# Kernel optimization log

Hardware: AMD Instinct MI355X
Metric: run time of the kernel (lower is better)

## Reference

```python
import jax, jax.numpy as jnp
import numpy as np

H = 4096  # hidden_size == input_size


def setup_inputs() -> dict:
    key = jax.random.key(0)
    ks = jax.random.split(key, 12)
    s = 0.02  # weight init scale
    return {
        "x": jax.random.normal(ks[0], (H,), jnp.float32),
        "h_prev": jnp.zeros((H,), jnp.float32),
        "C_prev": jax.random.normal(ks[1], (H, H), jnp.float32) * 0.01,
        "n_prev": jax.random.uniform(ks[2], (H,), jnp.float32) + 1.0,
        # projection weights (hidden_size x input_size) and biases
        "Wq": jax.random.normal(ks[3], (H, H), jnp.float32) * s,
        "Wk": jax.random.normal(ks[4], (H, H), jnp.float32) * s,
        "Wv": jax.random.normal(ks[5], (H, H), jnp.float32) * s,
        "Wo": jax.random.normal(ks[6], (H, H), jnp.float32) * s,
        "bq": jnp.zeros((H,), jnp.float32),
        "bk": jnp.zeros((H,), jnp.float32),
        "bv": jnp.zeros((H,), jnp.float32),
        "bo": jnp.zeros((H,), jnp.float32),
        # scalar input/forget gates: w^T x + b
        "wi": jax.random.normal(ks[7], (H,), jnp.float32) * s,
        "bi": jnp.zeros((), jnp.float32),
        "wf": jax.random.normal(ks[8], (H,), jnp.float32) * s,
        "bf": jnp.ones((), jnp.float32),  # bias forget gate toward remembering
    }


def reference(x, h_prev, C_prev, n_prev, Wq, Wk, Wv, Wo,
              bq, bk, bv, bo, wi, bi, wf, bf):
    # mLSTM single-step cell (xLSTM matrix memory). h_prev is unused by the
    # mLSTM math (no hidden-to-hidden recurrence), matching the CUDA layer API.
    d = jnp.asarray(Wk.shape[0], x.dtype)
    q = Wq @ x + bq                                   # [H]
    k = (Wk @ x + bk) / jnp.sqrt(d)                   # [H], scaled key
    v = Wv @ x + bv                                   # [H]
    i_gate = jnp.exp(jnp.dot(wi, x) + bi)             # scalar exponential input gate
    f_gate = jax.nn.sigmoid(jnp.dot(wf, x) + bf)      # scalar sigmoid forget gate
    # covariance-style rank-1 matrix-memory update
    C = f_gate * C_prev + i_gate * jnp.outer(v, k)    # [H, H]
    n = f_gate * n_prev + i_gate * k                  # [H]
    # normalized readout
    denom = jnp.maximum(jnp.abs(jnp.dot(n, q)), jnp.asarray(1.0, x.dtype))
    h_tilde = (C @ q) / denom                         # [H]
    o_gate = jax.nn.sigmoid(Wo @ x + bo)              # [H] output gate
    h = o_gate * h_tilde
    return (h, C, n)
```

## Files before the change

### kernel.cpp

```cpp
#include <hip/hip_runtime.h>
#include <math.h>

#define H 4096
#define H4 (H / 4)

typedef float f4 __attribute__((ext_vector_type(4)));

__device__ __forceinline__ float wave_reduce_sum(float v) {
    #pragma unroll
    for (int off = 32; off > 0; off >>= 1)
        v += __shfl_down(v, off, 64);
    return v;
}

__device__ __forceinline__ float sigmoidf_(float x) {
    return 1.0f / (1.0f + __expf(-x));
}

__device__ __forceinline__ float dot4(f4 a, f4 b) {
    return a.x * b.x + a.y * b.y + a.z * b.z + a.w * b.w;
}

__global__ __launch_bounds__(1024) void gemv_all(
    const float* __restrict__ x,
    const float* __restrict__ Wq, const float* __restrict__ Wk,
    const float* __restrict__ Wv, const float* __restrict__ Wo,
    const float* __restrict__ bq, const float* __restrict__ bk,
    const float* __restrict__ bv, const float* __restrict__ bo,
    const float* __restrict__ wi, const float* __restrict__ wf,
    float* __restrict__ q, float* __restrict__ k,
    float* __restrict__ v, float* __restrict__ og,
    float* __restrict__ s2)
{
    const int tid  = threadIdx.x;
    const int wave = tid >> 6;
    const int lane = tid & 63;

    __shared__ f4 xs[H4];
    const f4* x4 = (const f4*)x;
    xs[tid] = x4[tid];
    __syncthreads();

    const int rowId = blockIdx.x * 16 + wave;
    if (rowId >= 4 * H + 2) return;

    const int m = rowId >> 12;
    const int r = rowId & (H - 1);

    const float* row;
    if (rowId < 4 * H) {
        const float* W = (m == 0) ? Wq : (m == 1) ? Wk : (m == 2) ? Wv : Wo;
        row = W + (size_t)r * H;
    } else {
        row = (rowId == 4 * H) ? wi : wf;
    }
    const f4* row4 = (const f4*)row;

    float s = 0.0f;
    #pragma unroll
    for (int half = 0; half < 2; ++half) {
        const int base = half * 512;
        f4 a0 = __builtin_nontemporal_load(&row4[lane + base +   0]);
        f4 a1 = __builtin_nontemporal_load(&row4[lane + base +  64]);
        f4 a2 = __builtin_nontemporal_load(&row4[lane + base + 128]);
        f4 a3 = __builtin_nontemporal_load(&row4[lane + base + 192]);
        f4 a4_ = __builtin_nontemporal_load(&row4[lane + base + 256]);
        f4 a5 = __builtin_nontemporal_load(&row4[lane + base + 320]);
        f4 a6 = __builtin_nontemporal_load(&row4[lane + base + 384]);
        f4 a7 = __builtin_nontemporal_load(&row4[lane + base + 448]);
        s += dot4(a0,  xs[lane + base +   0]);
        s += dot4(a1,  xs[lane + base +  64]);
        s += dot4(a2,  xs[lane + base + 128]);
        s += dot4(a3,  xs[lane + base + 192]);
        s += dot4(a4_, xs[lane + base + 256]);
        s += dot4(a5,  xs[lane + base + 320]);
        s += dot4(a6,  xs[lane + base + 384]);
        s += dot4(a7,  xs[lane + base + 448]);
    }

    s = wave_reduce_sum(s);

    if (lane == 0) {
        if (rowId < 4 * H) {
            if (m == 0)      q[r]  = s + bq[r];
            else if (m == 1) k[r]  = (s + bk[r]) * 0.015625f;
            else if (m == 2) v[r]  = s + bv[r];
            else             og[r] = sigmoidf_(s + bo[r]);
        } else {
            s2[rowId - 4 * H] = s;
        }
    }
}

__global__ __launch_bounds__(256) void c_update(
    const float* __restrict__ C_prev,
    const float* __restrict__ q, const float* __restrict__ k,
    const float* __restrict__ v, const float* __restrict__ s2,
    const float* __restrict__ bi, const float* __restrict__ bf,
    float* __restrict__ C_out, float* __restrict__ u)
{
    const int tid  = threadIdx.x;
    const int wave = tid >> 6;
    const int lane = tid & 63;

    __shared__ f4 qs[H4];
    __shared__ f4 ks[H4];
    const f4* q4 = (const f4*)q;
    const f4* k4 = (const f4*)k;
    #pragma unroll
    for (int i = 0; i < 4; ++i) {
        qs[tid + i * 256] = q4[tid + i * 256];
        ks[tid + i * 256] = k4[tid + i * 256];
    }
    __syncthreads();

    const int r = blockIdx.x * 4 + wave;

    const float ig  = __expf(s2[0] + bi[0]);
    const float fg  = sigmoidf_(s2[1] + bf[0]);
    const float ivr = ig * v[r];

    const f4* c4 = (const f4*)(C_prev + (size_t)r * H);
    f4*       o4 = (f4*)(C_out + (size_t)r * H);

    float acc = 0.0f;
    #pragma unroll
    for (int half = 0; half < 2; ++half) {
        const int base = half * 512;
        f4 a0 = __builtin_nontemporal_load(&c4[lane + base +   0]);
        f4 a1 = __builtin_nontemporal_load(&c4[lane + base +  64]);
        f4 a2 = __builtin_nontemporal_load(&c4[lane + base + 128]);
        f4 a3 = __builtin_nontemporal_load(&c4[lane + base + 192]);
        f4 a4_ = __builtin_nontemporal_load(&c4[lane + base + 256]);
        f4 a5 = __builtin_nontemporal_load(&c4[lane + base + 320]);
        f4 a6 = __builtin_nontemporal_load(&c4[lane + base + 384]);
        f4 a7 = __builtin_nontemporal_load(&c4[lane + base + 448]);

        f4 o;
        #define CONSUME(reg, off)                                        \
            {                                                            \
                f4 kk = ks[lane + (off)];                                \
                o.x = fg * reg.x + ivr * kk.x;                           \
                o.y = fg * reg.y + ivr * kk.y;                           \
                o.z = fg * reg.z + ivr * kk.z;                           \
                o.w = fg * reg.w + ivr * kk.w;                           \
                __builtin_nontemporal_store(o, &o4[lane + (off)]);       \
                acc += dot4(reg, qs[lane + (off)]);                      \
            }
        CONSUME(a0, base +   0) CONSUME(a1, base +  64)
        CONSUME(a2, base + 128) CONSUME(a3, base + 192)
        CONSUME(a4_, base + 256) CONSUME(a5, base + 320)
        CONSUME(a6, base + 384) CONSUME(a7, base + 448)
        #undef CONSUME
    }

    acc = wave_reduce_sum(acc);
    if (lane == 0) u[r] = acc;
}

__global__ __launch_bounds__(1024) void finalize(
    const float* __restrict__ n_prev,
    const float* __restrict__ q, const float* __restrict__ k,
    const float* __restrict__ v, const float* __restrict__ og,
    const float* __restrict__ u, const float* __restrict__ s2,
    const float* __restrict__ bi, const float* __restrict__ bf,
    float* __restrict__ h, float* __restrict__ n_out)
{
    const int t = threadIdx.x;
    const int wave = t >> 6;
    const int lane = t & 63;

    const float ig = __expf(s2[0] + bi[0]);
    const float fg = sigmoidf_(s2[1] + bf[0]);

    float nq = 0.0f, kq = 0.0f;
    for (int j = t; j < H; j += 1024) {
        float kj = k[j];
        float qj = q[j];
        float nj = fg * n_prev[j] + ig * kj;
        n_out[j] = nj;
        nq += nj * qj;
        kq += kj * qj;
    }
    nq = wave_reduce_sum(nq);
    kq = wave_reduce_sum(kq);

    __shared__ float snq[16], skq[16];
    if (lane == 0) { snq[wave] = nq; skq[wave] = kq; }
    __syncthreads();
    if (t == 0) {
        float a = 0.0f, b = 0.0f;
        #pragma unroll
        for (int w = 0; w < 16; ++w) { a += snq[w]; b += skq[w]; }
        snq[0] = a; skq[0] = b;
    }
    __syncthreads();

    const float denom = fmaxf(fabsf(snq[0]), 1.0f);
    const float kqv = skq[0];
    const float inv_denom = 1.0f / denom;

    for (int j = t; j < H; j += 1024) {
        float ht = (fg * u[j] + ig * v[j] * kqv) * inv_denom;
        h[j] = og[j] * ht;
    }
}

extern "C" void kernel_launch(void* const* d_in, const int* in_sizes, int n_in,
                              void* d_out, int out_size, void* d_ws, size_t ws_size,
                              hipStream_t stream) {
    const float* x      = (const float*)d_in[0];
    const float* C_prev = (const float*)d_in[2];
    const float* n_prev = (const float*)d_in[3];
    const float* Wq     = (const float*)d_in[4];
    const float* Wk     = (const float*)d_in[5];
    const float* Wv     = (const float*)d_in[6];
    const float* Wo     = (const float*)d_in[7];
    const float* bq     = (const float*)d_in[8];
    const float* bk     = (const float*)d_in[9];
    const float* bv     = (const float*)d_in[10];
    const float* bo     = (const float*)d_in[11];
    const float* wi     = (const float*)d_in[12];
    const float* bi     = (const float*)d_in[13];
    const float* wf     = (const float*)d_in[14];
    const float* bf     = (const float*)d_in[15];

    float* out   = (float*)d_out;
    float* h_out = out;
    float* C_out = out + H;
    float* n_out = out + H + (size_t)H * H;

    float* ws = (float*)d_ws;
    float* q  = ws;
    float* k  = ws + H;
    float* v  = ws + 2 * H;
    float* og = ws + 3 * H;
    float* u  = ws + 4 * H;
    float* s2 = ws + 5 * H;

    const int nrows = 4 * H + 2;
    const int blocks1 = (nrows + 15) / 16;
    gemv_all<<<blocks1, 1024, 0, stream>>>(x, Wq, Wk, Wv, Wo, bq, bk, bv, bo,
                                           wi, wf, q, k, v, og, s2);

    c_update<<<H / 4, 256, 0, stream>>>(C_prev, q, k, v, s2, bi, bf, C_out, u);

    finalize<<<1, 1024, 0, stream>>>(n_prev, q, k, v, og, u, s2, bi, bf,
                                     h_out, n_out);
}
```

Baseline: 314.7 us.

## Move Wo GEMV into the C-update kernel to rebalance memory traffic

```diff
diff --git a/kernel.cpp b/kernel.cpp
--- a/kernel.cpp
+++ b/kernel.cpp
@@ -21,41 +21,9 @@
     return a.x * b.x + a.y * b.y + a.z * b.z + a.w * b.w;
 }
 
-__global__ __launch_bounds__(1024) void gemv_all(
-    const float* __restrict__ x,
-    const float* __restrict__ Wq, const float* __restrict__ Wk,
-    const float* __restrict__ Wv, const float* __restrict__ Wo,
-    const float* __restrict__ bq, const float* __restrict__ bk,
-    const float* __restrict__ bv, const float* __restrict__ bo,
-    const float* __restrict__ wi, const float* __restrict__ wf,
-    float* __restrict__ q, float* __restrict__ k,
-    float* __restrict__ v, float* __restrict__ og,
-    float* __restrict__ s2)
-{
-    const int tid  = threadIdx.x;
-    const int wave = tid >> 6;
-    const int lane = tid & 63;
-
-    __shared__ f4 xs[H4];
-    const f4* x4 = (const f4*)x;
-    xs[tid] = x4[tid];
-    __syncthreads();
-
-    const int rowId = blockIdx.x * 16 + wave;
-    if (rowId >= 4 * H + 2) return;
-
-    const int m = rowId >> 12;
-    const int r = rowId & (H - 1);
-
-    const float* row;
-    if (rowId < 4 * H) {
-        const float* W = (m == 0) ? Wq : (m == 1) ? Wk : (m == 2) ? Wv : Wo;
-        row = W + (size_t)r * H;
-    } else {
-        row = (rowId == 4 * H) ? wi : wf;
-    }
-    const f4* row4 = (const f4*)row;
-
+__device__ __forceinline__ float gemv_row_nt(const f4* __restrict__ row4,
+                                             const f4* __restrict__ xs,
+                                             int lane) {
     float s = 0.0f;
     #pragma unroll
     for (int half = 0; half < 2; ++half) {
@@ -77,85 +45,136 @@
         s += dot4(a6,  xs[lane + base + 384]);
         s += dot4(a7,  xs[lane + base + 448]);
     }
-
-    s = wave_reduce_sum(s);
-
-    if (lane == 0) {
-        if (rowId < 4 * H) {
-            if (m == 0)      q[r]  = s + bq[r];
-            else if (m == 1) k[r]  = (s + bk[r]) * 0.015625f;
-            else if (m == 2) v[r]  = s + bv[r];
-            else             og[r] = sigmoidf_(s + bo[r]);
-        } else {
-            s2[rowId - 4 * H] = s;
-        }
-    }
-}
-
-__global__ __launch_bounds__(256) void c_update(
-    const float* __restrict__ C_prev,
-    const float* __restrict__ q, const float* __restrict__ k,
-    const float* __restrict__ v, const float* __restrict__ s2,
-    const float* __restrict__ bi, const float* __restrict__ bf,
-    float* __restrict__ C_out, float* __restrict__ u)
+    return s;
+}
+
+__global__ __launch_bounds__(1024) void gemv_qkv(
+    const float* __restrict__ x,
+    const float* __restrict__ Wq, const float* __restrict__ Wk,
+    const float* __restrict__ Wv,
+    const float* __restrict__ bq, const float* __restrict__ bk,
+    const float* __restrict__ bv,
+    const float* __restrict__ wi, const float* __restrict__ wf,
+    float* __restrict__ q, float* __restrict__ k,
+    float* __restrict__ v, float* __restrict__ s2)
 {
     const int tid  = threadIdx.x;
     const int wave = tid >> 6;
     const int lane = tid & 63;
 
-    __shared__ f4 qs[H4];
-    __shared__ f4 ks[H4];
-    const f4* q4 = (const f4*)q;
-    const f4* k4 = (const f4*)k;
-    #pragma unroll
-    for (int i = 0; i < 4; ++i) {
-        qs[tid + i * 256] = q4[tid + i * 256];
-        ks[tid + i * 256] = k4[tid + i * 256];
-    }
+    __shared__ f4 xs[H4];
+    const f4* x4 = (const f4*)x;
+    xs[tid] = x4[tid];
     __syncthreads();
 
-    const int r = blockIdx.x * 4 + wave;
-
-    const float ig  = __expf(s2[0] + bi[0]);
-    const float fg  = sigmoidf_(s2[1] + bf[0]);
-    const float ivr = ig * v[r];
-
-    const f4* c4 = (const f4*)(C_prev + (size_t)r * H);
-    f4*       o4 = (f4*)(C_out + (size_t)r * H);
-
-    float acc = 0.0f;
-    #pragma unroll
-    for (int half = 0; half < 2; ++half) {
-        const int base = half * 512;
-        f4 a0 = __builtin_nontemporal_load(&c4[lane + base +   0]);
-        f4 a1 = __builtin_nontemporal_load(&c4[lane + base +  64]);
-        f4 a2 = __builtin_nontemporal_load(&c4[lane + base + 128]);
-        f4 a3 = __builtin_nontemporal_load(&c4[lane + base + 192]);
-        f4 a4_ = __builtin_nontemporal_load(&c4[lane + base + 256]);
-        f4 a5 = __builtin_nontemporal_load(&c4[lane + base + 320]);
-        f4 a6 = __builtin_nontemporal_load(&c4[lane + base + 384]);
-        f4 a7 = __builtin_nontemporal_load(&c4[lane + base + 448]);
-
-        f4 o;
-        #define CONSUME(reg, off)                                        \
-            {                                                            \
-                f4 kk = ks[lane + (off)];                                \
-                o.x = fg * reg.x + ivr * kk.x;                           \
-                o.y = fg * reg.y + ivr * kk.y;                           \
-                o.z = fg * reg.z + ivr * kk.z;                           \
-                o.w = fg * reg.w + ivr * kk.w;                           \
-                __builtin_nontemporal_store(o, &o4[lane + (off)]);       \
-                acc += dot4(reg, qs[lane + (off)]);                      \
-            }
-        CONSUME(a0, base +   0) CONSUME(a1, base +  64)
-        CONSUME(a2, base + 128) CONSUME(a3, base + 192)
-        CONSUME(a4_, base + 256) CONSUME(a5, base + 320)
-        CONSUME(a6, base + 384) CONSUME(a7, base + 448)
-        #undef CONSUME
-    }
-
-    acc = wave_reduce_sum(acc);
-    if (lane == 0) u[r] = acc;
+    const int rowId = blockIdx.x * 16 + wave;
+    if (rowId >= 3 * H + 2) return;
+
+    const int m = rowId >> 12;
+    const int r = rowId & (H - 1);
+
+    const float* row;
+    if (rowId < 3 * H) {
+        const float* W = (m == 0) ? Wq : (m == 1) ? Wk : Wv;
+        row = W + (size_t)r * H;
+    } else {
+        row = (rowId == 3 * H) ? wi : wf;
+    }
+
+    float s = gemv_row_nt((const f4*)row, xs, lane);
+    s = wave_reduce_sum(s);
+
+    if (lane == 0) {
+        if (rowId < 3 * H) {
+            if (m == 0)      q[r] = s + bq[r];
+            else if (m == 1) k[r] = (s + bk[r]) * 0.015625f;
+            else             v[r] = s + bv[r];
+        } else {
+            s2[rowId - 3 * H] = s;
+        }
+    }
+}
+
+__global__ __launch_bounds__(1024) void c_update_o(
+    const float* __restrict__ C_prev,
+    const float* __restrict__ x,
+    const float* __restrict__ Wo, const float* __restrict__ bo,
+    const float* __restrict__ q, const float* __restrict__ k,
+    const float* __restrict__ v, const float* __restrict__ s2,
+    const float* __restrict__ bi, const float* __restrict__ bf,
+    float* __restrict__ C_out, float* __restrict__ u,
+    float* __restrict__ og)
+{
+    const int tid  = threadIdx.x;
+    const int wave = tid >> 6;
+    const int lane = tid & 63;
+
+    __shared__ f4 lds[2 * H4];
+
+    if (blockIdx.x < H / 16) {
+        f4* qs = lds;
+        f4* ks = lds + H4;
+        const f4* q4 = (const f4*)q;
+        const f4* k4 = (const f4*)k;
+        qs[tid] = q4[tid];
+        ks[tid] = k4[tid];
+        __syncthreads();
+
+        const int r = blockIdx.x * 16 + wave;
+
+        const float ig  = __expf(s2[0] + bi[0]);
+        const float fg  = sigmoidf_(s2[1] + bf[0]);
+        const float ivr = ig * v[r];
+
+        const f4* c4 = (const f4*)(C_prev + (size_t)r * H);
+        f4*       o4 = (f4*)(C_out + (size_t)r * H);
+
+        float acc = 0.0f;
+        #pragma unroll
+        for (int half = 0; half < 2; ++half) {
+            const int base = half * 512;
+            f4 a0 = __builtin_nontemporal_load(&c4[lane + base +   0]);
+            f4 a1 = __builtin_nontemporal_load(&c4[lane + base +  64]);
+            f4 a2 = __builtin_nontemporal_load(&c4[lane + base + 128]);
+            f4 a3 = __builtin_nontemporal_load(&c4[lane + base + 192]);
+            f4 a4_ = __builtin_nontemporal_load(&c4[lane + base + 256]);
+            f4 a5 = __builtin_nontemporal_load(&c4[lane + base + 320]);
+            f4 a6 = __builtin_nontemporal_load(&c4[lane + base + 384]);
+            f4 a7 = __builtin_nontemporal_load(&c4[lane + base + 448]);
+
+            f4 o;
+            #define CONSUME(reg, off)                                    \
+                {                                                        \
+                    f4 kk = ks[lane + (off)];                            \
+                    o.x = fg * reg.x + ivr * kk.x;                       \
+                    o.y = fg * reg.y + ivr * kk.y;                       \
+                    o.z = fg * reg.z + ivr * kk.z;                       \
+                    o.w = fg * reg.w + ivr * kk.w;                       \
+                    __builtin_nontemporal_store(o, &o4[lane + (off)]);   \
+                    acc += dot4(reg, qs[lane + (off)]);                  \
+                }
+            CONSUME(a0, base +   0) CONSUME(a1, base +  64)
+            CONSUME(a2, base + 128) CONSUME(a3, base + 192)
+            CONSUME(a4_, base + 256) CONSUME(a5, base + 320)
+            CONSUME(a6, base + 384) CONSUME(a7, base + 448)
+            #undef CONSUME
+        }
+
+        acc = wave_reduce_sum(acc);
+        if (lane == 0) u[r] = acc;
+    } else {
+        f4* xs = lds;
+        const f4* x4 = (const f4*)x;
+        xs[tid] = x4[tid];
+        __syncthreads();
+
+        const int r = (blockIdx.x - H / 16) * 16 + wave;
+        const f4* row4 = (const f4*)(Wo + (size_t)r * H);
+
+        float s = gemv_row_nt(row4, xs, lane);
+        s = wave_reduce_sum(s);
+        if (lane == 0) og[r] = sigmoidf_(s + bo[r]);
+    }
 }
 
 __global__ __launch_bounds__(1024) void finalize(
@@ -238,12 +257,14 @@
     float* u  = ws + 4 * H;
     float* s2 = ws + 5 * H;
 
-    const int nrows = 4 * H + 2;
-    const int blocks1 = (nrows + 15) / 16;
-    gemv_all<<<blocks1, 1024, 0, stream>>>(x, Wq, Wk, Wv, Wo, bq, bk, bv, bo,
-                                           wi, wf, q, k, v, og, s2);
-
-    c_update<<<H / 4, 256, 0, stream>>>(C_prev, q, k, v, s2, bi, bf, C_out, u);
+    const int nrows1 = 3 * H + 2;
+    const int blocks1 = (nrows1 + 15) / 16;
+    gemv_qkv<<<blocks1, 1024, 0, stream>>>(x, Wq, Wk, Wv, bq, bk, bv,
+                                           wi, wf, q, k, v, s2);
+
+    c_update_o<<<2 * (H / 16), 1024, 0, stream>>>(C_prev, x, Wo, bo,
+                                                  q, k, v, s2, bi, bf,
+                                                  C_out, u, og);
 
     finalize<<<1, 1024, 0, stream>>>(n_prev, q, k, v, og, u, s2, bi, bf,
                                      h_out, n_out);
```

After: 317.4 us. Within noise of the previous version (+0.9%).
